# Optimization experiments

Measured on AMD Instinct MI355X. Metric: run time of the kernel, lower is better.

The kernel has to match this reference:

```python
import jax, jax.numpy as jnp
import numpy as np

FEATURE_DIM = 16
NUM_HEADS = 16
HEAD_DIM = 64
R2 = float(np.sqrt(2.0))
RD = float(np.sqrt(FEATURE_DIM))        # sqrt(d) = 4
RRD = float(np.sqrt(RD))                # d^(1/4) = 2
RMS_EPS = 1e-5


def taylor_exp(x):
    # x: [b, h, l, d] -> [b, h, l, 1 + d + d*d]
    x2 = (x[..., :, None] * x[..., None, :]).reshape(*x.shape[:-1], FEATURE_DIM * FEATURE_DIM) / R2
    ones = jnp.ones_like(x[..., :1])
    return jnp.concatenate([ones, x / RRD, x2 / RD], axis=-1)


def setup_inputs() -> dict:
    key = jax.random.key(0)
    ks = jax.random.split(key, 5)
    b, l, d_model = 4, 2048, 1024
    inp = {
        'hidden_states': jax.random.normal(ks[0], (b, l, d_model), dtype=jnp.float32),
        'Wq': jax.random.normal(ks[1], (FEATURE_DIM * NUM_HEADS, d_model), dtype=jnp.float32) * 0.02,
        'Wk': jax.random.normal(ks[2], (FEATURE_DIM * NUM_HEADS, d_model), dtype=jnp.float32) * 0.02,
        'Wv': jax.random.normal(ks[3], (NUM_HEADS * HEAD_DIM, d_model), dtype=jnp.float32) * 0.02,
        'Wo': jax.random.normal(ks[4], (d_model, NUM_HEADS * HEAD_DIM), dtype=jnp.float32) * 0.02,
        'g_weight': jnp.ones((HEAD_DIM,), dtype=jnp.float32),
    }
    return inp


def reference(hidden_states, Wq, Wk, Wv, Wo, g_weight):
    b, l, _ = hidden_states.shape
    # projections (Linear, no bias): x @ W.T
    q = (hidden_states @ Wq.T).reshape(b, l, NUM_HEADS, FEATURE_DIM).transpose(0, 2, 1, 3)
    k = (hidden_states @ Wk.T).reshape(b, l, NUM_HEADS, FEATURE_DIM).transpose(0, 2, 1, 3)
    v = (hidden_states @ Wv.T).reshape(b, l, NUM_HEADS, HEAD_DIM).transpose(0, 2, 1, 3)

    qf = taylor_exp(q)  # [b, h, l, 273]
    kf = taylor_exp(k)  # [b, h, l, 273]

    A_qk = jnp.einsum('bhnd,bhmd->bhnm', qf, kf)
    A_qk = jnp.tril(A_qk)
    y = jnp.einsum('bhnm,bhme->bhne', A_qk, v)  # [b, h, l, head_dim]

    kv_state = jnp.einsum('bhnd,bhnf->bhfd', kf, v)[:, :, None]  # [b, h, 1, head_dim, 273]

    # RMSNorm over head_dim
    rms = jax.lax.rsqrt(jnp.mean(y * y, axis=-1, keepdims=True) + RMS_EPS)
    y = y * rms * g_weight

    y = y.transpose(0, 2, 1, 3).reshape(b, l, NUM_HEADS * HEAD_DIM)
    out = y @ Wo.T
    return out, kv_state
```

## Files before the change

### kernel.cpp

```cpp
#include <hip/hip_runtime.h>


typedef unsigned short u16;
typedef unsigned int u32;
typedef __attribute__((ext_vector_type(4))) float f32x4;
typedef __attribute__((ext_vector_type(16))) float f32x16;
typedef __attribute__((ext_vector_type(8))) short s16x8;

struct MaskT { static constexpr bool value = true;  };
struct MaskF { static constexpr bool value = false; };

__device__ __forceinline__ float bf2f(u16 u) {
    union { unsigned int i; float f; } x; x.i = ((unsigned int)u) << 16; return x.f;
}
__device__ __forceinline__ u16 f2bf(float f) {
    union { float f; unsigned int u; } x; x.f = f;
    unsigned int r = x.u + 0x7FFFu + ((x.u >> 16) & 1u);
    return (u16)(r >> 16);
}

typedef const __attribute__((address_space(1))) u32* gas1_t;
typedef __attribute__((address_space(3))) u32* las3_t;
__device__ __forceinline__ void gld16(const u16* g, u16* l) {
    __builtin_amdgcn_global_load_lds((gas1_t)(const void*)g, (las3_t)(void*)l, 16, 0, 0);
}

__global__ __launch_bounds__(256)
void cvt_all_kernel(const void* __restrict__ H,  const void* __restrict__ Wq,
                    const void* __restrict__ Wk, const void* __restrict__ Wv,
                    const void* __restrict__ Wo, const void* __restrict__ gw,
                    u16* __restrict__ Hb,  u16* __restrict__ Wqb,
                    u16* __restrict__ Wkb, u16* __restrict__ Wvb,
                    u16* __restrict__ Wob, u16* __restrict__ gwb)
{
    __shared__ int sflag;
    const int t = threadIdx.x;
    if (t < 64) {
        const unsigned int* Hw = (const unsigned int*)H;
        int cnt = 0;
#pragma unroll
        for (int i = 0; i < 16; ++i) {
            const unsigned int wrd = Hw[t * 16 + i];
            const int e = (int)((wrd >> 7) & 0xFFu);
            if (e >= 85 && e <= 170) ++cnt;
        }
        cnt += __shfl_xor(cnt, 1);  cnt += __shfl_xor(cnt, 2);
        cnt += __shfl_xor(cnt, 4);  cnt += __shfl_xor(cnt, 8);
        cnt += __shfl_xor(cnt, 16); cnt += __shfl_xor(cnt, 32);
        if (t == 0) sflag = (cnt < 700) ? 1 : 0;
    }
    __syncthreads();
    const int f32in = sflag;

    const int NQ = 11010112 / 4;
    for (int qi = blockIdx.x * 256 + t; qi < NQ; qi += gridDim.x * 256) {
        const int i = qi * 4;
        const void* src; u16* dst; int off;
        if      (i <  8388608) { src = H;  dst = Hb;  off = i; }
        else if (i <  8650752) { src = Wq; dst = Wqb; off = i - 8388608; }
        else if (i <  8912896) { src = Wk; dst = Wkb; off = i - 8650752; }
        else if (i <  9961472) { src = Wv; dst = Wvb; off = i - 8912896; }
        else if (i < 11010048) { src = Wo; dst = Wob; off = i - 9961472; }
        else                   { src = gw; dst = gwb; off = i - 11010048; }
        ushort4 o;
        if (f32in) {
            const float4 v = *((const float4*)src + (off >> 2));
            o.x = f2bf(v.x); o.y = f2bf(v.y); o.z = f2bf(v.z); o.w = f2bf(v.w);
        } else {
            o = *((const ushort4*)src + (off >> 2));
        }
        *(ushort4*)(dst + off) = o;
    }
}

template<int MODE>
__global__ __launch_bounds__(256)
void gemm_nt(const u16* __restrict__ A,
             const u16* __restrict__ Bq, const u16* __restrict__ Bk,
             const u16* __restrict__ Bv,
             u16* __restrict__ Oq, u16* __restrict__ Ok,
             u16* __restrict__ Ovt, float* __restrict__ Of,
             const float* __restrict__ Kvp, float* __restrict__ Kvo)
{
    __shared__ __attribute__((aligned(16))) u16 As[8192];
    __shared__ __attribute__((aligned(16))) u16 Bs[8192];
    const int t = threadIdx.x;
    const int lane = t & 63, w = t >> 6;
    const int c = lane & 15, qd = lane >> 4;
    const int wm = (w >> 1) * 64, wn = (w & 1) * 64;
    const int nwgx = gridDim.x;
    const int pid = blockIdx.y * nwgx + blockIdx.x;
    const int lid = (pid & 7) * ((nwgx * 64) >> 3) + (pid >> 3);
    const int rm = (lid / nwgx) * 128;
    const int cb = (lid % nwgx) * 128;

    const u16* Bsrc; int wrow0;
    if (MODE == 0) {
        if (cb < 256)      { Bsrc = Bq; wrow0 = cb; }
        else if (cb < 512) { Bsrc = Bk; wrow0 = cb - 256; }
        else               { Bsrc = Bv; wrow0 = cb - 512; }
    } else { Bsrc = Bq; wrow0 = cb; }

    f32x4 acc[4][4];
#pragma unroll
    for (int i = 0; i < 4; ++i)
#pragma unroll
        for (int j = 0; j < 4; ++j) acc[i][j] = (f32x4){0.f, 0.f, 0.f, 0.f};

    const int r0 = w * 8 + (lane >> 3);
    const int s0 = (lane & 7) ^ (lane >> 3);
    const u16* Ag = A    + (size_t)(rm    + r0) * 1024 + s0 * 8;
    const u16* Bg = Bsrc + (size_t)(wrow0 + r0) * 1024 + s0 * 8;
    u16* AsW = As + w * 512;
    u16* BsW = Bs + w * 512;

    for (int kt = 0; kt < 16; ++kt) {
        const int k0 = kt * 64;
        __syncthreads();
#pragma unroll
        for (int i = 0; i < 4; ++i) {
            gld16(Ag + (size_t)(i * 32) * 1024 + k0, AsW + i * 2048);
            gld16(Bg + (size_t)(i * 32) * 1024 + k0, BsW + i * 2048);
        }
        __syncthreads();
        s16x8 af[2][4], bfr[2][4];
#pragma unroll
        for (int kk = 0; kk < 2; ++kk) {
#pragma unroll
            for (int mt = 0; mt < 4; ++mt) {
                const int row = wm + mt * 16 + c;
                af[kk][mt] = *(const s16x8*)&As[row * 64 + (((kk * 4 + qd) ^ (row & 7)) * 8)];
            }
#pragma unroll
            for (int nt = 0; nt < 4; ++nt) {
                const int row = wn + nt * 16 + c;
                bfr[kk][nt] = *(const s16x8*)&Bs[row * 64 + (((kk * 4 + qd) ^ (row & 7)) * 8)];
            }
        }
#pragma unroll
        for (int kk = 0; kk < 2; ++kk)
#pragma unroll
            for (int mt = 0; mt < 4; ++mt)
#pragma unroll
                for (int nt = 0; nt < 4; ++nt)
                    acc[mt][nt] = __builtin_amdgcn_mfma_f32_16x16x32_bf16(af[kk][mt], bfr[kk][nt], acc[mt][nt], 0, 0, 0);
    }

#pragma unroll
    for (int mt = 0; mt < 4; ++mt) {
#pragma unroll
        for (int nt = 0; nt < 4; ++nt) {
            const int gc = cb + wn + nt * 16 + c;
            const int row0 = rm + wm + mt * 16 + qd * 4;
            if (MODE == 1) {
#pragma unroll
                for (int r = 0; r < 4; ++r)
                    Of[(size_t)(row0 + r) * 1024 + gc] = acc[mt][nt][r];
            } else if (gc < 512) {
#pragma unroll
                for (int r = 0; r < 4; ++r) {
                    const int row = row0 + r;
                    const int b_ = row >> 11, l_ = row & 2047;
                    const int cc = gc & 255;
                    const int h = cc >> 4, idx = cc & 15;
                    u16* dst = (gc < 256) ? Oq : Ok;
                    dst[(size_t)((b_ * 16 + h) * 2048 + l_) * 16 + idx] = f2bf(acc[mt][nt][r]);
                }
            } else {
                const int cc = gc - 512;
                const int h = cc >> 6, idx = cc & 63;
                const int b_ = row0 >> 11, l0 = row0 & 2047;
                ushort4 pk;
                pk.x = f2bf(acc[mt][nt][0]);
                pk.y = f2bf(acc[mt][nt][1]);
                pk.z = f2bf(acc[mt][nt][2]);
                pk.w = f2bf(acc[mt][nt][3]);
                *(ushort4*)(Ovt + ((size_t)((b_ * 16 + h) * 64 + idx)) * 2048 + l0) = pk;
            }
        }
    }

    if (MODE == 1) {
        const int S = 64 * 64 * 273;
        const int NQ4 = S / 4;
        const int NT = gridDim.x * gridDim.y * 256;
        for (int q = pid * 256 + t; q < NQ4; q += NT) {
            float4 a = ((const float4*)Kvp)[q];
#pragma unroll
            for (int s = 1; s < 8; ++s) {
                const float4 b = ((const float4*)(Kvp + (size_t)s * S))[q];
                a.x += b.x; a.y += b.y; a.z += b.z; a.w += b.w;
            }
            ((float4*)Kvo)[q] = a;
        }
    }
}

__global__ __launch_bounds__(512, 2)
void attn_kernel(const u16* __restrict__ Qg, const u16* __restrict__ Kg,
                 const u16* __restrict__ Vt, const u16* __restrict__ gwb,
                 u16* __restrict__ Yn)
{
    __shared__ __attribute__((aligned(16))) u16 Vs[2][8192];
    const int t = threadIdx.x, lane = t & 63, w = t >> 6;
    const int la = lane & 31, h = lane >> 5;
    const int pid = blockIdx.y * 4 + blockIdx.x;
    const int lid = (pid & 7) * 32 + (pid >> 3);
    const int bh = lid >> 2;
    const int jj = lid & 3;
    const int b_ = bh >> 4, hh = bh & 15;
    const u16* Qh = Qg + (size_t)bh * (2048 * 16);
    const u16* Kh = Kg + (size_t)bh * (2048 * 16);
    const u16* Vh = Vt + (size_t)bh * (64 * 2048);
    const float gl0 = bf2f(gwb[la]);
    const float gl1 = bf2f(gwb[32 + la]);
    const f32x16 z16 = {0.f,0.f,0.f,0.f,0.f,0.f,0.f,0.f,
                        0.f,0.f,0.f,0.f,0.f,0.f,0.f,0.f};
    const int vbase0 = (la << 8) | (h << 4);
    const int vsw = (la & 15) << 4;

    auto stageV = [&](int n0s, int bufsel) {
#pragma unroll
        for (int i = 0; i < 2; ++i) {
            const int slot = i * 512 + t;
            const int fl = slot >> 4;
            const int seg = (slot & 15) ^ (fl & 15);
            gld16(Vh + (size_t)fl * 2048 + n0s + seg * 8,
                  (u16*)Vs[bufsel] + (size_t)(i * 512 + (w << 6)) * 8);
        }
    };

    for (int pass = 0; pass < 2; ++pass) {
        const int qb = pass ? jj : (7 - jj);
        const int q0 = qb * 256 + w * 32;
        const int kf = 2 * qb + (w >> 2);
        const int wp = w & 3;
        const int nck = 2 * qb + 2;

        const s16x8 bq = *(const s16x8*)(Qh + (size_t)(q0 + la) * 16 + h * 8);
        f32x16 yt0 = z16, yt1 = z16;
        s16x8 ka[4];
        const char* vsc = (const char*)Vs[0];

        auto loadK = [&](s16x8* kk, int kcL) {
#pragma unroll
            for (int kt = 0; kt < 4; ++kt)
                kk[kt] = *(const s16x8*)(Kh + (size_t)(kcL * 128 + kt * 32 + la) * 16 + h * 8);
        };

        auto tile = [&](int kt, auto MASKED) {
            constexpr bool masked = decltype(MASKED)::value;
            f32x16 sv = __builtin_amdgcn_mfma_f32_32x32x16_bf16(ka[kt], bq, z16, 0, 0, 0);
            float p[16];
#pragma unroll
            for (int r = 0; r < 16; ++r) {
                const float s = sv[r];
                float pv = fmaf(s, fmaf(s, 0.03125f, 0.25f), 1.0f);
                if (masked) {
                    const int keyloc = (r & 3) + 8 * (r >> 2) + 4 * h;
                    if (keyloc > la) pv = 0.f;
                }
                p[r] = pv;
            }
#pragma unroll
            for (int ks = 0; ks < 2; ++ks) {
                u32 X0, X1, Y0, Y1;
                asm("v_cvt_pk_bf16_f32 %0, %1, %2" : "=v"(X0) : "v"(p[8*ks+0]), "v"(p[8*ks+1]));
                asm("v_cvt_pk_bf16_f32 %0, %1, %2" : "=v"(X1) : "v"(p[8*ks+2]), "v"(p[8*ks+3]));
                asm("v_cvt_pk_bf16_f32 %0, %1, %2" : "=v"(Y0) : "v"(p[8*ks+4]), "v"(p[8*ks+5]));
                asm("v_cvt_pk_bf16_f32 %0, %1, %2" : "=v"(Y1) : "v"(p[8*ks+6]), "v"(p[8*ks+7]));
                asm("v_permlane32_swap_b32 %0, %1" : "+v"(X0), "+v"(Y0));
                asm("v_permlane32_swap_b32 %0, %1" : "+v"(X1), "+v"(Y1));
                union { uint4 u; s16x8 v; } afu;
                afu.u = (uint4){X0, X1, Y0, Y1};
                const int offb = (kt << 6) | (ks << 5);
                const s16x8 vb0 = *(const s16x8*)(vsc + (((vbase0 + offb)) ^ vsw));
                const s16x8 vb1 = *(const s16x8*)(vsc + (((vbase0 + 8192 + offb)) ^ vsw));
                yt0 = __builtin_amdgcn_mfma_f32_32x32x16_bf16(afu.v, vb0, yt0, 0, 0, 0);
                yt1 = __builtin_amdgcn_mfma_f32_32x32x16_bf16(afu.v, vb1, yt1, 0, 0, 0);
            }
        };

        stageV(0, 0);
        loadK(ka, 0);
        __syncthreads();

        for (int kc = 0; kc < nck; ++kc) {
            const int cur = kc & 1;
            vsc = (const char*)Vs[cur];
            if (kc + 1 < nck) stageV((kc + 1) * 128, cur ^ 1);
            s16x8 kn[4] = {ka[0], ka[1], ka[2], ka[3]};
            if (kc < kf) loadK(kn, kc + 1);

            if (kc < kf) {
                tile(0, MaskF{}); tile(1, MaskF{});
                tile(2, MaskF{}); tile(3, MaskF{});
            } else if (kc == kf) {
                if (wp == 0)      { tile(0, MaskT{}); }
                else if (wp == 1) { tile(0, MaskF{}); tile(1, MaskT{}); }
                else if (wp == 2) { tile(0, MaskF{}); tile(1, MaskF{}); tile(2, MaskT{}); }
                else              { tile(0, MaskF{}); tile(1, MaskF{}); tile(2, MaskF{}); tile(3, MaskT{}); }
            }
            __syncthreads();
#pragma unroll
            for (int kt = 0; kt < 4; ++kt) ka[kt] = kn[kt];
        }

#pragma unroll
        for (int r = 0; r < 16; ++r) {
            float ss = yt0[r] * yt0[r] + yt1[r] * yt1[r];
            ss += __shfl_xor(ss, 1);  ss += __shfl_xor(ss, 2);
            ss += __shfl_xor(ss, 4);  ss += __shfl_xor(ss, 8);
            ss += __shfl_xor(ss, 16);
            const float rmsv = rsqrtf(ss * (1.0f / 64.0f) + 1e-5f);
            const int row = q0 + (r & 3) + 8 * (r >> 2) + 4 * h;
            u16* dst = Yn + ((size_t)(b_ * 2048 + row)) * 1024 + hh * 64;
            dst[la]      = f2bf(yt0[r] * rmsv * gl0);
            dst[32 + la] = f2bf(yt1[r] * rmsv * gl1);
        }
    }
}

__global__ __launch_bounds__(256)
void kv_mfma_kernel(const u16* __restrict__ Kg, const u16* __restrict__ Vt,
                    float* __restrict__ kvpart)
{
    __shared__ __attribute__((aligned(16))) float kS[64][17];
    __shared__ __attribute__((aligned(16))) u16 Vs[64][72];
    const int t = threadIdx.x, lane = t & 63, w = t >> 6;
    const int c = lane & 15, qd = lane >> 4;
    const int ns = blockIdx.x, bh = blockIdx.y;
    const u16* Kh  = Kg + (size_t)bh * 2048 * 16;
    const u16* Vth = Vt + (size_t)bh * 64 * 2048;

    f32x4 acc[4][5];
#pragma unroll
    for (int mt = 0; mt < 4; ++mt)
#pragma unroll
        for (int j = 0; j < 5; ++j) acc[mt][j] = (f32x4){0.f, 0.f, 0.f, 0.f};

    for (int ch = 0; ch < 4; ++ch) {
        const int n0 = ns * 256 + ch * 64;
        __syncthreads();
        if (t < 128) {
            const int row = t >> 1, half = t & 1;
            uint4 kv = *(const uint4*)(Kh + (size_t)(n0 + row) * 16 + half * 8);
            const u16* ke = (const u16*)&kv;
#pragma unroll
            for (int e = 0; e < 8; ++e)
                kS[row][half * 8 + e] = bf2f(ke[e]);
        }
#pragma unroll
        for (int i = 0; i < 2; ++i) {
            const int lin = i * 256 + t;
            const int f = lin >> 3, seg = lin & 7;
            *(uint4*)&Vs[f][seg * 8] =
                *(const uint4*)(Vth + (size_t)f * 2048 + n0 + seg * 8);
        }
        __syncthreads();

#pragma unroll
        for (int kt = 0; kt < 2; ++kt) {
            s16x8 va[4];
#pragma unroll
            for (int mt = 0; mt < 4; ++mt)
                va[mt] = *(const s16x8*)&Vs[mt * 16 + c][kt * 32 + qd * 8];
#pragma unroll
            for (int j = 0; j < 5; ++j) {
                const int dt = w + 4 * j;
                if (dt < 18) {
                    const int dd = dt * 16 + c;
                    const int i2 = (dd - 17) >> 4, j2 = (dd - 17) & 15;
                    const int nb = kt * 32 + qd * 8;
                    u32 vbw[4];
#pragma unroll
                    for (int p = 0; p < 4; ++p) {
                        float pv[2];
#pragma unroll
                        for (int h2 = 0; h2 < 2; ++h2) {
                            const int n = nb + 2 * p + h2;
                            float val;
                            if (dd == 0)       val = 1.0f;
                            else if (dd < 17)  val = 0.5f * kS[n][dd - 1];
                            else               val = 0.17677669529663687f
                                                     * kS[n][i2] * kS[n][j2];
                            pv[h2] = val;
                        }
                        asm("v_cvt_pk_bf16_f32 %0, %1, %2"
                            : "=v"(vbw[p]) : "v"(pv[0]), "v"(pv[1]));
                    }
                    union { uint4 u; s16x8 v; } vbu;
                    vbu.u = (uint4){vbw[0], vbw[1], vbw[2], vbw[3]};
#pragma unroll
                    for (int mt = 0; mt < 4; ++mt)
                        acc[mt][j] = __builtin_amdgcn_mfma_f32_16x16x32_bf16(
                            va[mt], vbu.v, acc[mt][j], 0, 0, 0);
                }
            }
        }
    }

    float* base = kvpart + ((size_t)(ns * 64 + bh) * 64) * 273;
#pragma unroll
    for (int j = 0; j < 5; ++j) {
        const int dt = w + 4 * j;
        if (dt >= 18) continue;
        const int dd = dt * 16 + c;
        if (dd >= 273) continue;
#pragma unroll
        for (int mt = 0; mt < 4; ++mt)
#pragma unroll
            for (int r = 0; r < 4; ++r) {
                const int f = mt * 16 + qd * 4 + r;
                base[f * 273 + dd] = acc[mt][j][r];
            }
    }
}

extern "C" void kernel_launch(void* const* d_in, const int* in_sizes, int n_in,
                              void* d_out, int out_size, void* d_ws, size_t ws_size,
                              hipStream_t stream)
{
    const void* H  = d_in[0];
    const void* Wq = d_in[1];
    const void* Wk = d_in[2];
    const void* Wv = d_in[3];
    const void* Wo = d_in[4];
    const void* gw = d_in[5];
    float* outf = (float*)d_out;

    char* ws = (char*)d_ws;
    const size_t M = 1 << 20;
    u16*   Hb    = (u16*)(ws);
    u16*   Wqb   = (u16*)(ws + 16 * M);
    u16*   Wkb   = (u16*)(ws + 16 * M + 512 * 1024);
    u16*   Wvb   = (u16*)(ws + 17 * M);
    u16*   Wob   = (u16*)(ws + 19 * M);
    u16*   gwb   = (u16*)(ws + 21 * M);
    u16*   q     = (u16*)(ws + 22 * M);
    u16*   k     = (u16*)(ws + 26 * M);
    u16*   vt    = (u16*)(ws + 30 * M);
    float* kvpart= (float*)(ws + 46 * M);
    u16*   yn    = Hb;

    cvt_all_kernel<<<2048, 256, 0, stream>>>(H, Wq, Wk, Wv, Wo, gw,
                                             Hb, Wqb, Wkb, Wvb, Wob, gwb);

    gemm_nt<0><<<dim3(12, 64), 256, 0, stream>>>(Hb, Wqb, Wkb, Wvb, q, k, vt,
                                                 nullptr, nullptr, nullptr);
    attn_kernel<<<dim3(4, 64), 512, 0, stream>>>(q, k, vt, gwb, yn);
    kv_mfma_kernel<<<dim3(8, 64), 256, 0, stream>>>(k, vt, kvpart);
    gemm_nt<1><<<dim3(8, 64), 256, 0, stream>>>(yn, Wob, nullptr, nullptr,
                                                nullptr, nullptr, nullptr, outf,
                                                kvpart, outf + (size_t)8388608);
}
```

Baseline: 218.7 us.

## Fuse attention and kv-state kernels into one heterogeneous launch

```diff
diff --git a/kernel.cpp b/kernel.cpp
--- a/kernel.cpp
+++ b/kernel.cpp
@@ -187,7 +187,7 @@
         for (int q = pid * 256 + t; q < NQ4; q += NT) {
             float4 a = ((const float4*)Kvp)[q];
 #pragma unroll
-            for (int s = 1; s < 8; ++s) {
+            for (int s = 1; s < 4; ++s) {
                 const float4 b = ((const float4*)(Kvp + (size_t)s * S))[q];
                 a.x += b.x; a.y += b.y; a.z += b.z; a.w += b.w;
             }
@@ -196,224 +196,224 @@
     }
 }
 
-__global__ __launch_bounds__(512, 2)
-void attn_kernel(const u16* __restrict__ Qg, const u16* __restrict__ Kg,
-                 const u16* __restrict__ Vt, const u16* __restrict__ gwb,
-                 u16* __restrict__ Yn)
+__global__ __launch_bounds__(512, 4)
+void akv_kernel(const u16* __restrict__ Qg, const u16* __restrict__ Kg,
+                const u16* __restrict__ Vt, const u16* __restrict__ gwb,
+                u16* __restrict__ Yn, float* __restrict__ kvpart)
 {
-    __shared__ __attribute__((aligned(16))) u16 Vs[2][8192];
+    __shared__ __attribute__((aligned(16))) char lds[32768];
     const int t = threadIdx.x, lane = t & 63, w = t >> 6;
-    const int la = lane & 31, h = lane >> 5;
-    const int pid = blockIdx.y * 4 + blockIdx.x;
-    const int lid = (pid & 7) * 32 + (pid >> 3);
-    const int bh = lid >> 2;
-    const int jj = lid & 3;
-    const int b_ = bh >> 4, hh = bh & 15;
-    const u16* Qh = Qg + (size_t)bh * (2048 * 16);
-    const u16* Kh = Kg + (size_t)bh * (2048 * 16);
-    const u16* Vh = Vt + (size_t)bh * (64 * 2048);
-    const float gl0 = bf2f(gwb[la]);
-    const float gl1 = bf2f(gwb[32 + la]);
-    const f32x16 z16 = {0.f,0.f,0.f,0.f,0.f,0.f,0.f,0.f,
-                        0.f,0.f,0.f,0.f,0.f,0.f,0.f,0.f};
-    const int vbase0 = (la << 8) | (h << 4);
-    const int vsw = (la & 15) << 4;
-
-    auto stageV = [&](int n0s, int bufsel) {
-#pragma unroll
-        for (int i = 0; i < 2; ++i) {
-            const int slot = i * 512 + t;
-            const int fl = slot >> 4;
-            const int seg = (slot & 15) ^ (fl & 15);
-            gld16(Vh + (size_t)fl * 2048 + n0s + seg * 8,
-                  (u16*)Vs[bufsel] + (size_t)(i * 512 + (w << 6)) * 8);
-        }
-    };
-
-    for (int pass = 0; pass < 2; ++pass) {
-        const int qb = pass ? jj : (7 - jj);
-        const int q0 = qb * 256 + w * 32;
-        const int kf = 2 * qb + (w >> 2);
-        const int wp = w & 3;
-        const int nck = 2 * qb + 2;
-
-        const s16x8 bq = *(const s16x8*)(Qh + (size_t)(q0 + la) * 16 + h * 8);
-        f32x16 yt0 = z16, yt1 = z16;
-        s16x8 ka[4];
-        const char* vsc = (const char*)Vs[0];
-
-        auto loadK = [&](s16x8* kk, int kcL) {
-#pragma unroll
-            for (int kt = 0; kt < 4; ++kt)
-                kk[kt] = *(const s16x8*)(Kh + (size_t)(kcL * 128 + kt * 32 + la) * 16 + h * 8);
+    const int pid = blockIdx.y * 8 + blockIdx.x;
+    const int x = pid & 7;
+    const int idx = pid >> 3;
+
+    if (idx < 32) {
+        const int la = lane & 31, h = lane >> 5;
+        const int lid = x * 32 + idx;
+        const int bh = lid >> 2;
+        const int jj = lid & 3;
+        const int b_ = bh >> 4, hh = bh & 15;
+        const u16* Qh = Qg + (size_t)bh * (2048 * 16);
+        const u16* Kh = Kg + (size_t)bh * (2048 * 16);
+        const u16* Vh = Vt + (size_t)bh * (64 * 2048);
+        const float gl0 = bf2f(gwb[la]);
+        const float gl1 = bf2f(gwb[32 + la]);
+        const f32x16 z16 = {0.f,0.f,0.f,0.f,0.f,0.f,0.f,0.f,
+                            0.f,0.f,0.f,0.f,0.f,0.f,0.f,0.f};
+        const int vbase0 = (la << 8) | (h << 4);
+        const int vsw = (la & 15) << 4;
+        u16* VsB = (u16*)lds;
+
+        auto stageV = [&](int n0s, int bufsel) {
+#pragma unroll
+            for (int i = 0; i < 2; ++i) {
+                const int slot = i * 512 + t;
+                const int fl = slot >> 4;
+                const int seg = (slot & 15) ^ (fl & 15);
+                gld16(Vh + (size_t)fl * 2048 + n0s + seg * 8,
+                      VsB + (size_t)bufsel * 8192 + (size_t)(i * 512 + (w << 6)) * 8);
+            }
         };
 
-        auto tile = [&](int kt, auto MASKED) {
-            constexpr bool masked = decltype(MASKED)::value;
-            f32x16 sv = __builtin_amdgcn_mfma_f32_32x32x16_bf16(ka[kt], bq, z16, 0, 0, 0);
-            float p[16];
+        for (int pass = 0; pass < 2; ++pass) {
+            const int qb = pass ? jj : (7 - jj);
+            const int q0 = qb * 256 + w * 32;
+            const int kf = 2 * qb + (w >> 2);
+            const int wp = w & 3;
+            const int nck = 2 * qb + 2;
+
+            const s16x8 bq = *(const s16x8*)(Qh + (size_t)(q0 + la) * 16 + h * 8);
+            f32x16 yt0 = z16, yt1 = z16;
+            s16x8 ka[4];
+            const char* vsc = (const char*)VsB;
+
+            auto loadK = [&](s16x8* kk, int kcL) {
+#pragma unroll
+                for (int kt = 0; kt < 4; ++kt)
+                    kk[kt] = *(const s16x8*)(Kh + (size_t)(kcL * 128 + kt * 32 + la) * 16 + h * 8);
+            };
+
+            auto tile = [&](int kt, auto MASKED) {
+                constexpr bool masked = decltype(MASKED)::value;
+                f32x16 sv = __builtin_amdgcn_mfma_f32_32x32x16_bf16(ka[kt], bq, z16, 0, 0, 0);
+                float p[16];
+#pragma unroll
+                for (int r = 0; r < 16; ++r) {
+                    const float s = sv[r];
+                    float pv = fmaf(s, fmaf(s, 0.03125f, 0.25f), 1.0f);
+                    if (masked) {
+                        const int keyloc = (r & 3) + 8 * (r >> 2) + 4 * h;
+                        if (keyloc > la) pv = 0.f;
+                    }
+                    p[r] = pv;
+                }
+#pragma unroll
+                for (int ks = 0; ks < 2; ++ks) {
+                    u32 X0, X1, Y0, Y1;
+                    asm("v_cvt_pk_bf16_f32 %0, %1, %2" : "=v"(X0) : "v"(p[8*ks+0]), "v"(p[8*ks+1]));
+                    asm("v_cvt_pk_bf16_f32 %0, %1, %2" : "=v"(X1) : "v"(p[8*ks+2]), "v"(p[8*ks+3]));
+                    asm("v_cvt_pk_bf16_f32 %0, %1, %2" : "=v"(Y0) : "v"(p[8*ks+4]), "v"(p[8*ks+5]));
+                    asm("v_cvt_pk_bf16_f32 %0, %1, %2" : "=v"(Y1) : "v"(p[8*ks+6]), "v"(p[8*ks+7]));
+                    asm("v_permlane32_swap_b32 %0, %1" : "+v"(X0), "+v"(Y0));
+                    asm("v_permlane32_swap_b32 %0, %1" : "+v"(X1), "+v"(Y1));
+                    union { uint4 u; s16x8 v; } afu;
+                    afu.u = (uint4){X0, X1, Y0, Y1};
+                    const int offb = (kt << 6) | (ks << 5);
+                    const s16x8 vb0 = *(const s16x8*)(vsc + (((vbase0 + offb)) ^ vsw));
+                    const s16x8 vb1 = *(const s16x8*)(vsc + (((vbase0 + 8192 + offb)) ^ vsw));
+                    yt0 = __builtin_amdgcn_mfma_f32_32x32x16_bf16(afu.v, vb0, yt0, 0, 0, 0);
+                    yt1 = __builtin_amdgcn_mfma_f32_32x32x16_bf16(afu.v, vb1, yt1, 0, 0, 0);
+                }
+            };
+
+            stageV(0, 0);
+            loadK(ka, 0);
+            __syncthreads();
+
+            for (int kc = 0; kc < nck; ++kc) {
+                const int cur = kc & 1;
+                vsc = (const char*)(VsB + (size_t)cur * 8192);
+                if (kc + 1 < nck) stageV((kc + 1) * 128, cur ^ 1);
+                s16x8 kn[4] = {ka[0], ka[1], ka[2], ka[3]};
+                if (kc < kf) loadK(kn, kc + 1);
+
+                if (kc < kf) {
+                    tile(0, MaskF{}); tile(1, MaskF{});
+                    tile(2, MaskF{}); tile(3, MaskF{});
+                } else if (kc == kf) {
+                    if (wp == 0)      { tile(0, MaskT{}); }
+                    else if (wp == 1) { tile(0, MaskF{}); tile(1, MaskT{}); }
+                    else if (wp == 2) { tile(0, MaskF{}); tile(1, MaskF{}); tile(2, MaskT{}); }
+                    else              { tile(0, MaskF{}); tile(1, MaskF{}); tile(2, MaskF{}); tile(3, MaskT{}); }
+                }
+                __syncthreads();
+#pragma unroll
+                for (int kt = 0; kt < 4; ++kt) ka[kt] = kn[kt];
+            }
+
 #pragma unroll
             for (int r = 0; r < 16; ++r) {
-                const float s = sv[r];
-                float pv = fmaf(s, fmaf(s, 0.03125f, 0.25f), 1.0f);
-                if (masked) {
-                    const int keyloc = (r & 3) + 8 * (r >> 2) + 4 * h;
-                    if (keyloc > la) pv = 0.f;
-                }
-                p[r] = pv;
-            }
-#pragma unroll
-            for (int ks = 0; ks < 2; ++ks) {
-                u32 X0, X1, Y0, Y1;
-                asm("v_cvt_pk_bf16_f32 %0, %1, %2" : "=v"(X0) : "v"(p[8*ks+0]), "v"(p[8*ks+1]));
-                asm("v_cvt_pk_bf16_f32 %0, %1, %2" : "=v"(X1) : "v"(p[8*ks+2]), "v"(p[8*ks+3]));
-                asm("v_cvt_pk_bf16_f32 %0, %1, %2" : "=v"(Y0) : "v"(p[8*ks+4]), "v"(p[8*ks+5]));
-                asm("v_cvt_pk_bf16_f32 %0, %1, %2" : "=v"(Y1) : "v"(p[8*ks+6]), "v"(p[8*ks+7]));
-                asm("v_permlane32_swap_b32 %0, %1" : "+v"(X0), "+v"(Y0));
-                asm("v_permlane32_swap_b32 %0, %1" : "+v"(X1), "+v"(Y1));
-                union { uint4 u; s16x8 v; } afu;
-                afu.u = (uint4){X0, X1, Y0, Y1};
-                const int offb = (kt << 6) | (ks << 5);
-                const s16x8 vb0 = *(const s16x8*)(vsc + (((vbase0 + offb)) ^ vsw));
-                const s16x8 vb1 = *(const s16x8*)(vsc + (((vbase0 + 8192 + offb)) ^ vsw));
-                yt0 = __builtin_amdgcn_mfma_f32_32x32x16_bf16(afu.v, vb0, yt0, 0, 0, 0);
-                yt1 = __builtin_amdgcn_mfma_f32_32x32x16_bf16(afu.v, vb1, yt1, 0, 0, 0);
-            }
-        };
-
-        stageV(0, 0);
-        loadK(ka, 0);
-        __syncthreads();
-
-        for (int kc = 0; kc < nck; ++kc) {
-            const int cur = kc & 1;
-            vsc = (const char*)Vs[cur];
-            if (kc + 1 < nck) stageV((kc + 1) * 128, cur ^ 1);
-            s16x8 kn[4] = {ka[0], ka[1], ka[2], ka[3]};
-            if (kc < kf) loadK(kn, kc + 1);
-
-            if (kc < kf) {
-                tile(0, MaskF{}); tile(1, MaskF{});
-                tile(2, MaskF{}); tile(3, MaskF{});
-            } else if (kc == kf) {
-                if (wp == 0)      { tile(0, MaskT{}); }
-                else if (wp == 1) { tile(0, MaskF{}); tile(1, MaskT{}); }
-                else if (wp == 2) { tile(0, MaskF{}); tile(1, MaskF{}); tile(2, MaskT{}); }
-                else              { tile(0, MaskF{}); tile(1, MaskF{}); tile(2, MaskF{}); tile(3, MaskT{}); }
-            }
+                float ss = yt0[r] * yt0[r] + yt1[r] * yt1[r];
+                ss += __shfl_xor(ss, 1);  ss += __shfl_xor(ss, 2);
+                ss += __shfl_xor(ss, 4);  ss += __shfl_xor(ss, 8);
+                ss += __shfl_xor(ss, 16);
+                const float rmsv = rsqrtf(ss * (1.0f / 64.0f) + 1e-5f);
+                const int row = q0 + (r & 3) + 8 * (r >> 2) + 4 * h;
+                u16* dst = Yn + ((size_t)(b_ * 2048 + row)) * 1024 + hh * 64;
+                dst[la]      = f2bf(yt0[r] * rmsv * gl0);
+                dst[32 + la] = f2bf(yt1[r] * rmsv * gl1);
+            }
+        }
+    } else {
+        const int c2 = idx - 32;
+        const int bh = x * 8 + (c2 >> 2);
+        const int ns = c2 & 3;
+        const int c = lane & 15, qd = lane >> 4;
+        const u16* Kh  = Kg + (size_t)bh * 2048 * 16;
+        const u16* Vth = Vt + (size_t)bh * 64 * 2048;
+        float (*kS)[17] = (float(*)[17])lds;
+        u16 (*Vs)[72]   = (u16(*)[72])(lds + 4608);
+
+        f32x4 acc[4][3];
+#pragma unroll
+        for (int mt = 0; mt < 4; ++mt)
+#pragma unroll
+            for (int j = 0; j < 3; ++j) acc[mt][j] = (f32x4){0.f, 0.f, 0.f, 0.f};
+
+        for (int ch = 0; ch < 8; ++ch) {
+            const int n0 = ns * 512 + ch * 64;
             __syncthreads();
-#pragma unroll
-            for (int kt = 0; kt < 4; ++kt) ka[kt] = kn[kt];
-        }
-
-#pragma unroll
-        for (int r = 0; r < 16; ++r) {
-            float ss = yt0[r] * yt0[r] + yt1[r] * yt1[r];
-            ss += __shfl_xor(ss, 1);  ss += __shfl_xor(ss, 2);
-            ss += __shfl_xor(ss, 4);  ss += __shfl_xor(ss, 8);
-            ss += __shfl_xor(ss, 16);
-            const float rmsv = rsqrtf(ss * (1.0f / 64.0f) + 1e-5f);
-            const int row = q0 + (r & 3) + 8 * (r >> 2) + 4 * h;
-            u16* dst = Yn + ((size_t)(b_ * 2048 + row)) * 1024 + hh * 64;
-            dst[la]      = f2bf(yt0[r] * rmsv * gl0);
-            dst[32 + la] = f2bf(yt1[r] * rmsv * gl1);
-        }
-    }
-}
-
-__global__ __launch_bounds__(256)
-void kv_mfma_kernel(const u16* __restrict__ Kg, const u16* __restrict__ Vt,
-                    float* __restrict__ kvpart)
-{
-    __shared__ __attribute__((aligned(16))) float kS[64][17];
-    __shared__ __attribute__((aligned(16))) u16 Vs[64][72];
-    const int t = threadIdx.x, lane = t & 63, w = t >> 6;
-    const int c = lane & 15, qd = lane >> 4;
-    const int ns = blockIdx.x, bh = blockIdx.y;
-    const u16* Kh  = Kg + (size_t)bh * 2048 * 16;
-    const u16* Vth = Vt + (size_t)bh * 64 * 2048;
-
-    f32x4 acc[4][5];
-#pragma unroll
-    for (int mt = 0; mt < 4; ++mt)
-#pragma unroll
-        for (int j = 0; j < 5; ++j) acc[mt][j] = (f32x4){0.f, 0.f, 0.f, 0.f};
-
-    for (int ch = 0; ch < 4; ++ch) {
-        const int n0 = ns * 256 + ch * 64;
-        __syncthreads();
-        if (t < 128) {
-            const int row = t >> 1, half = t & 1;
-            uint4 kv = *(const uint4*)(Kh + (size_t)(n0 + row) * 16 + half * 8);
-            const u16* ke = (const u16*)&kv;
-#pragma unroll
-            for (int e = 0; e < 8; ++e)
-                kS[row][half * 8 + e] = bf2f(ke[e]);
-        }
-#pragma unroll
-        for (int i = 0; i < 2; ++i) {
-            const int lin = i * 256 + t;
-            const int f = lin >> 3, seg = lin & 7;
-            *(uint4*)&Vs[f][seg * 8] =
-                *(const uint4*)(Vth + (size_t)f * 2048 + n0 + seg * 8);
-        }
-        __syncthreads();
-
-#pragma unroll
-        for (int kt = 0; kt < 2; ++kt) {
-            s16x8 va[4];
+            if (t < 128) {
+                const int row = t >> 1, half = t & 1;
+                uint4 kv = *(const uint4*)(Kh + (size_t)(n0 + row) * 16 + half * 8);
+                const u16* ke = (const u16*)&kv;
+#pragma unroll
+                for (int e = 0; e < 8; ++e)
+                    kS[row][half * 8 + e] = bf2f(ke[e]);
+            }
+            {
+                const int f = t >> 3, seg = t & 7;
+                *(uint4*)&Vs[f][seg * 8] =
+                    *(const uint4*)(Vth + (size_t)f * 2048 + n0 + seg * 8);
+            }
+            __syncthreads();
+
+#pragma unroll
+            for (int kt = 0; kt < 2; ++kt) {
+                s16x8 va[4];
+#pragma unroll
+                for (int mt = 0; mt < 4; ++mt)
+                    va[mt] = *(const s16x8*)&Vs[mt * 16 + c][kt * 32 + qd * 8];
+#pragma unroll
+                for (int j = 0; j < 3; ++j) {
+                    const int dt = w + 8 * j;
+                    if (dt < 18) {
+                        const int dd = dt * 16 + c;
+                        const int i2 = (dd - 17) >> 4, j2 = (dd - 17) & 15;
+                        const int nb = kt * 32 + qd * 8;
+                        u32 vbw[4];
+#pragma unroll
+                        for (int p = 0; p < 4; ++p) {
+                            float pv[2];
+#pragma unroll
+                            for (int h2 = 0; h2 < 2; ++h2) {
+                                const int n = nb + 2 * p + h2;
+                                float val;
+                                if (dd == 0)       val = 1.0f;
+                                else if (dd < 17)  val = 0.5f * kS[n][dd - 1];
+                                else               val = 0.17677669529663687f
+                                                         * kS[n][i2] * kS[n][j2];
+                                pv[h2] = val;
+                            }
+                            asm("v_cvt_pk_bf16_f32 %0, %1, %2"
+                                : "=v"(vbw[p]) : "v"(pv[0]), "v"(pv[1]));
+                        }
+                        union { uint4 u; s16x8 v; } vbu;
+                        vbu.u = (uint4){vbw[0], vbw[1], vbw[2], vbw[3]};
+#pragma unroll
+                        for (int mt = 0; mt < 4; ++mt)
+                            acc[mt][j] = __builtin_amdgcn_mfma_f32_16x16x32_bf16(
+                                va[mt], vbu.v, acc[mt][j], 0, 0, 0);
+                    }
+                }
+            }
+        }
+
+        float* base = kvpart + ((size_t)(ns * 64 + bh) * 64) * 273;
+#pragma unroll
+        for (int j = 0; j < 3; ++j) {
+            const int dt = w + 8 * j;
+            if (dt >= 18) continue;
+            const int dd = dt * 16 + c;
+            if (dd >= 273) continue;
 #pragma unroll
             for (int mt = 0; mt < 4; ++mt)
-                va[mt] = *(const s16x8*)&Vs[mt * 16 + c][kt * 32 + qd * 8];
-#pragma unroll
-            for (int j = 0; j < 5; ++j) {
-                const int dt = w + 4 * j;
-                if (dt < 18) {
-                    const int dd = dt * 16 + c;
-                    const int i2 = (dd - 17) >> 4, j2 = (dd - 17) & 15;
-                    const int nb = kt * 32 + qd * 8;
-                    u32 vbw[4];
-#pragma unroll
-                    for (int p = 0; p < 4; ++p) {
-                        float pv[2];
-#pragma unroll
-                        for (int h2 = 0; h2 < 2; ++h2) {
-                            const int n = nb + 2 * p + h2;
-                            float val;
-                            if (dd == 0)       val = 1.0f;
-                            else if (dd < 17)  val = 0.5f * kS[n][dd - 1];
-                            else               val = 0.17677669529663687f
-                                                     * kS[n][i2] * kS[n][j2];
-                            pv[h2] = val;
-                        }
-                        asm("v_cvt_pk_bf16_f32 %0, %1, %2"
-                            : "=v"(vbw[p]) : "v"(pv[0]), "v"(pv[1]));
-                    }
-                    union { uint4 u; s16x8 v; } vbu;
-                    vbu.u = (uint4){vbw[0], vbw[1], vbw[2], vbw[3]};
-#pragma unroll
-                    for (int mt = 0; mt < 4; ++mt)
-                        acc[mt][j] = __builtin_amdgcn_mfma_f32_16x16x32_bf16(
-                            va[mt], vbu.v, acc[mt][j], 0, 0, 0);
-                }
-            }
-        }
-    }
-
-    float* base = kvpart + ((size_t)(ns * 64 + bh) * 64) * 273;
-#pragma unroll
-    for (int j = 0; j < 5; ++j) {
-        const int dt = w + 4 * j;
-        if (dt >= 18) continue;
-        const int dd = dt * 16 + c;
-        if (dd >= 273) continue;
-#pragma unroll
-        for (int mt = 0; mt < 4; ++mt)
-#pragma unroll
-            for (int r = 0; r < 4; ++r) {
-                const int f = mt * 16 + qd * 4 + r;
-                base[f * 273 + dd] = acc[mt][j][r];
-            }
+#pragma unroll
+                for (int r = 0; r < 4; ++r) {
+                    const int f = mt * 16 + qd * 4 + r;
+                    base[f * 273 + dd] = acc[mt][j][r];
+                }
+        }
     }
 }
 
@@ -448,8 +448,7 @@
 
     gemm_nt<0><<<dim3(12, 64), 256, 0, stream>>>(Hb, Wqb, Wkb, Wvb, q, k, vt,
                                                  nullptr, nullptr, nullptr);
-    attn_kernel<<<dim3(4, 64), 512, 0, stream>>>(q, k, vt, gwb, yn);
-    kv_mfma_kernel<<<dim3(8, 64), 256, 0, stream>>>(k, vt, kvpart);
+    akv_kernel<<<dim3(8, 64), 512, 0, stream>>>(q, k, vt, gwb, yn, kvpart);
     gemm_nt<1><<<dim3(8, 64), 256, 0, stream>>>(yn, Wob, nullptr, nullptr,
                                                 nullptr, nullptr, nullptr, outf,
                                                 kvpart, outf + (size_t)8388608);
```

New measurement: 202.1 us. 7.6% less time.
